# Optimization experiments

Measured on AMD Instinct MI355X. Metric: run time of the kernel, lower is better.

## Reference

```python
import jax, jax.numpy as jnp
from jax import lax
import numpy as np

B, T, I, H, O = 64, 4096, 128, 256, 1

def setup_inputs() -> dict:
    key = jax.random.key(0)
    ks = jax.random.split(key, 6)
    x = jax.random.normal(ks[0], (B, T, I), dtype=jnp.float32)
    # Linear params with torch-style fan_in init scale
    Wd = jax.random.uniform(ks[1], (H, I), jnp.float32, -1.0, 1.0) / np.sqrt(I)
    bd = jax.random.uniform(ks[2], (H,), jnp.float32, -1.0, 1.0) / np.sqrt(I)
    Wo = jax.random.uniform(ks[3], (O, H), jnp.float32, -1.0, 1.0) / np.sqrt(H)
    bo = jax.random.uniform(ks[4], (O,), jnp.float32, -1.0, 1.0) / np.sqrt(H)
    tau = jnp.ones((H,), jnp.float32) * 2.0
    return {"x": x, "Wd": Wd, "bd": bd, "Wo": Wo, "bo": bo, "tau": tau}

def reference(x, Wd, bd, Wo, bo, tau):
    # precompute dense projection for all timesteps: [B,T,H]
    cur = jnp.einsum('bti,hi->bth', x, Wd) + bd
    alpha = jax.nn.sigmoid(tau)  # [H], per-channel decay
    mem0 = jnp.zeros((x.shape[0], tau.shape[0]), dtype=x.dtype)

    def step(mem, c_t):  # c_t: [B,H]
        mem = alpha * mem + (1.0 - alpha) * c_t
        return mem, mem

    _, mems = lax.scan(step, mem0, jnp.swapaxes(cur, 0, 1))  # mems: [T,B,H]
    mems = jnp.swapaxes(mems, 0, 1)  # [B,T,H]
    out = jax.nn.sigmoid(jnp.einsum('bth,oh->bto', mems, Wo) + bo)  # [B,T,O]
    return out
```

## Files before the change

kernel.cpp:

```cpp
#include <hip/hip_runtime.h>
#include <hip/hip_bf16.h>
#include <math.h>

#define BB 64
#define TT 4096
#define II 128
#define HH 256
#define DD 64
#define LL 128
#define NC (TT/LL)

typedef __attribute__((ext_vector_type(8))) short short8;
typedef __attribute__((ext_vector_type(4))) float f32x4;

__device__ inline ushort f2b(float f) {
    __hip_bfloat16 h = __float2bfloat16(f);
    return *reinterpret_cast<ushort*>(&h);
}

__global__ __launch_bounds__(256) void k0_tables(
    const float* __restrict__ Wd, const float* __restrict__ bd,
    const float* __restrict__ Wo, const float* __restrict__ bo,
    const float* __restrict__ tau,
    ushort* __restrict__ U, float* __restrict__ ybias)
{
    __shared__ float pw[HH];
    __shared__ float wb[HH];
    __shared__ float red[II];
    const int tid = threadIdx.x;
    const int blk = blockIdx.x;

    if (blk < DD) {
        const int d = blk;
        {
            float a = 1.0f / (1.0f + expf(-tau[tid]));
            pw[tid] = Wo[tid] * (1.0f - a) * exp2f((float)d * log2f(a));
        }
        __syncthreads();
        const int i = tid & 127, p = tid >> 7;
        float s = 0.0f;
#pragma unroll 8
        for (int hh = 0; hh < 128; ++hh) {
            int h = p * 128 + hh;
            s += pw[h] * Wd[h * II + i];
        }
        if (p) red[i] = s;
        __syncthreads();
        if (!p) U[d * II + i] = f2b(s + red[i]);
    } else {
        {
            float a = 1.0f / (1.0f + expf(-tau[tid]));
            pw[tid] = log2f(a);
            wb[tid] = Wo[tid] * bd[tid];
        }
        __syncthreads();
        const int t = (blk - DD) * 16 + (tid >> 4);
        const int hp = tid & 15;
        float s = 0.0f;
#pragma unroll
        for (int hh = 0; hh < 16; ++hh) {
            int h = hp * 16 + hh;
            s += wb[h] * (1.0f - exp2f((float)(t + 1) * pw[h]));
        }
#pragma unroll
        for (int m = 1; m < 16; m <<= 1) s += __shfl_xor(s, m, 64);
        if (hp == 0) ybias[t] = s + bo[0];
    }
}

__global__ __launch_bounds__(512, 8) void k1_conv(
    const float* __restrict__ x, const ushort* __restrict__ U,
    const float* __restrict__ ybias,
    float* __restrict__ fix, float* __restrict__ spill,
    float* __restrict__ out)
{
    __shared__ __align__(16) char smem[34048];
    float* P    = reinterpret_cast<float*>(smem);
    float* psum = reinterpret_cast<float*>(smem + 33280);

    const int b = blockIdx.x >> 5, tc = blockIdx.x & 31;
    const int t0 = tc * LL;
    const int tid  = threadIdx.x;
    const int lane = tid & 63, w = tid >> 6;
    const int l15  = lane & 15, quad = lane >> 4;

    const float4* xg = reinterpret_cast<const float4*>(x + ((size_t)b * TT + t0) * II);
#pragma unroll
    for (int it = 0; it < 4; ++it) {
        int c = it * 512 + tid;
        int r = c >> 4, ib = c & 15;
        float4 v0 = xg[r * 32 + ib * 2];
        float4 v1 = xg[r * 32 + ib * 2 + 1];
        short8 pk;
        ushort* pu = reinterpret_cast<ushort*>(&pk);
        pu[0] = f2b(v0.x); pu[1] = f2b(v0.y); pu[2] = f2b(v0.z); pu[3] = f2b(v0.w);
        pu[4] = f2b(v1.x); pu[5] = f2b(v1.y); pu[6] = f2b(v1.z); pu[7] = f2b(v1.w);
        int byte = (r << 8) + (ib << 4);
        byte ^= (r & 7) << 4;
        *reinterpret_cast<short8*>(smem + byte) = pk;
    }
    __syncthreads();

    const int nt = w & 3, mg = w >> 2;
    f32x4 acc[4];
#pragma unroll
    for (int mi = 0; mi < 4; ++mi) acc[mi] = (f32x4){0.f, 0.f, 0.f, 0.f};
#pragma unroll
    for (int kt = 0; kt < 4; ++kt) {
        short8 bfrag = *reinterpret_cast<const short8*>(
            &U[(nt * 16 + l15) * II + kt * 32 + quad * 8]);
#pragma unroll
        for (int mi = 0; mi < 4; ++mi) {
            int row  = (mg * 4 + mi) * 16 + l15;
            int byte = (row << 8) + kt * 64 + quad * 16;
            byte ^= (row & 7) << 4;
            short8 afrag = *reinterpret_cast<const short8*>(smem + byte);
            acc[mi] = __builtin_amdgcn_mfma_f32_16x16x32_bf16(afrag, bfrag, acc[mi], 0, 0, 0);
        }
    }
    __syncthreads();

#pragma unroll
    for (int mi = 0; mi < 4; ++mi)
#pragma unroll
        for (int rr = 0; rr < 4; ++rr)
            P[((mg * 4 + mi) * 16 + quad * 4 + rr) * 65 + nt * 16 + l15] = acc[mi][rr];
    __syncthreads();

    const int g = tid >> 8;
    const int j = tid & 255;
    float part = 0.0f;
    if (j < 192) {
#pragma unroll
        for (int i = 0; i < 32; ++i) {
            int d = g * 32 + i;
            int r = j - d;
            int rc = r < 0 ? 0 : (r > 127 ? 127 : r);
            float v = P[rc * 65 + d];
            part += (r == rc) ? v : 0.0f;
        }
        if (g) psum[j] = part;
    }
    __syncthreads();
    if (!g && j < 192) {
        float tot = part + psum[j];
        if (j < 63) {
            fix[((size_t)b * NC + tc) * 64 + j] = tot;
        } else if (j < 128) {
            int t = t0 + j;
            float yb = ybias[t < 128 ? t : 127];
            out[(size_t)b * TT + t] = 1.0f / (1.0f + expf(-(tot + yb)));
        } else {
            spill[((size_t)b * NC + tc) * 64 + (j - 128)] = tot;
        }
    }
}

__global__ __launch_bounds__(256) void k2_out(
    const float* __restrict__ fix, const float* __restrict__ spill,
    const float* __restrict__ ybias, float* __restrict__ out)
{
    int idx = blockIdx.x * 256 + threadIdx.x;
    int j = idx & 63, tc = (idx >> 6) & 31, b = idx >> 11;
    if (j >= 63) return;
    float v = fix[((size_t)b * NC + tc) * 64 + j];
    if (tc) v += spill[((size_t)b * NC + tc - 1) * 64 + j];
    int t = tc * LL + j;
    v += ybias[t < 128 ? t : 127];
    out[(size_t)b * TT + t] = 1.0f / (1.0f + expf(-v));
}

extern "C" void kernel_launch(void* const* d_in, const int* in_sizes, int n_in,
                              void* d_out, int out_size, void* d_ws, size_t ws_size,
                              hipStream_t stream) {
    const float* x   = (const float*)d_in[0];
    const float* Wd  = (const float*)d_in[1];
    const float* bd  = (const float*)d_in[2];
    const float* Wo  = (const float*)d_in[3];
    const float* bo  = (const float*)d_in[4];
    const float* tau = (const float*)d_in[5];
    float* out = (float*)d_out;

    float* ws = (float*)d_ws;
    float*  ybias = ws;
    ushort* U     = (ushort*)(ws + 128);
    float*  fix   = ws + 128 + 4096;
    float*  spill = fix + BB * NC * 64;

    k0_tables<<<72, 256, 0, stream>>>(Wd, bd, Wo, bo, tau, U, ybias);
    k1_conv<<<BB * NC, 512, 0, stream>>>(x, U, ybias, fix, spill, out);
    k2_out<<<512, 256, 0, stream>>>(fix, spill, ybias, out);
}
```

Before: 213.6 us.

## Load x fragments directly to registers and reduce diagonals with LDS atomics

The conv kernel no longer stages the bf16 x tile in shared memory. Each wave loads its own 16-row A fragments straight from global memory into registers and loops over all four U column tiles. The staged P matrix and the diagonal gather pass are replaced by shared-memory atomicAdd into a 192-entry accumulator indexed by row+d. This removes LDS traffic and two barriers, but adds 16 LDS atomics per thread, and contention on those atomics could serialize.

```diff
diff --git a/kernel.cpp b/kernel.cpp
--- a/kernel.cpp
+++ b/kernel.cpp
@@ -74,9 +74,7 @@
     float* __restrict__ fix, float* __restrict__ spill,
     float* __restrict__ out)
 {
-    __shared__ __align__(16) char smem[34048];
-    float* P    = reinterpret_cast<float*>(smem);
-    float* psum = reinterpret_cast<float*>(smem + 33280);
+    __shared__ float yacc[192];
 
     const int b = blockIdx.x >> 5, tc = blockIdx.x & 31;
     const int t0 = tc * LL;
@@ -84,66 +82,44 @@
     const int lane = tid & 63, w = tid >> 6;
     const int l15  = lane & 15, quad = lane >> 4;
 
-    const float4* xg = reinterpret_cast<const float4*>(x + ((size_t)b * TT + t0) * II);
+    if (tid < 192) yacc[tid] = 0.0f;
+
+    const float* xr = x + ((size_t)b * TT + t0 + w * 16 + l15) * II + quad * 8;
+    short8 af[4];
 #pragma unroll
-    for (int it = 0; it < 4; ++it) {
-        int c = it * 512 + tid;
-        int r = c >> 4, ib = c & 15;
-        float4 v0 = xg[r * 32 + ib * 2];
-        float4 v1 = xg[r * 32 + ib * 2 + 1];
-        short8 pk;
-        ushort* pu = reinterpret_cast<ushort*>(&pk);
+    for (int kt = 0; kt < 4; ++kt) {
+        float4 v0 = *reinterpret_cast<const float4*>(xr + kt * 32);
+        float4 v1 = *reinterpret_cast<const float4*>(xr + kt * 32 + 4);
+        ushort* pu = reinterpret_cast<ushort*>(&af[kt]);
         pu[0] = f2b(v0.x); pu[1] = f2b(v0.y); pu[2] = f2b(v0.z); pu[3] = f2b(v0.w);
         pu[4] = f2b(v1.x); pu[5] = f2b(v1.y); pu[6] = f2b(v1.z); pu[7] = f2b(v1.w);
-        int byte = (r << 8) + (ib << 4);
-        byte ^= (r & 7) << 4;
-        *reinterpret_cast<short8*>(smem + byte) = pk;
     }
+
     __syncthreads();
 
-    const int nt = w & 3, mg = w >> 2;
     f32x4 acc[4];
 #pragma unroll
-    for (int mi = 0; mi < 4; ++mi) acc[mi] = (f32x4){0.f, 0.f, 0.f, 0.f};
+    for (int nt = 0; nt < 4; ++nt) acc[nt] = (f32x4){0.f, 0.f, 0.f, 0.f};
+    const ushort* Ub = U + (size_t)l15 * II + quad * 8;
 #pragma unroll
-    for (int kt = 0; kt < 4; ++kt) {
-        short8 bfrag = *reinterpret_cast<const short8*>(
-            &U[(nt * 16 + l15) * II + kt * 32 + quad * 8]);
+    for (int nt = 0; nt < 4; ++nt)
 #pragma unroll
-        for (int mi = 0; mi < 4; ++mi) {
-            int row  = (mg * 4 + mi) * 16 + l15;
-            int byte = (row << 8) + kt * 64 + quad * 16;
-            byte ^= (row & 7) << 4;
-            short8 afrag = *reinterpret_cast<const short8*>(smem + byte);
-            acc[mi] = __builtin_amdgcn_mfma_f32_16x16x32_bf16(afrag, bfrag, acc[mi], 0, 0, 0);
+        for (int kt = 0; kt < 4; ++kt) {
+            short8 bf = *reinterpret_cast<const short8*>(Ub + (nt * 16) * II + kt * 32);
+            acc[nt] = __builtin_amdgcn_mfma_f32_16x16x32_bf16(af[kt], bf, acc[nt], 0, 0, 0);
         }
-    }
+
+    const int jb = w * 16 + quad * 4 + l15;
+#pragma unroll
+    for (int nt = 0; nt < 4; ++nt)
+#pragma unroll
+        for (int rr = 0; rr < 4; ++rr)
+            atomicAdd(&yacc[jb + nt * 16 + rr], acc[nt][rr]);
     __syncthreads();
 
-#pragma unroll
-    for (int mi = 0; mi < 4; ++mi)
-#pragma unroll
-        for (int rr = 0; rr < 4; ++rr)
-            P[((mg * 4 + mi) * 16 + quad * 4 + rr) * 65 + nt * 16 + l15] = acc[mi][rr];
-    __syncthreads();
-
-    const int g = tid >> 8;
-    const int j = tid & 255;
-    float part = 0.0f;
-    if (j < 192) {
-#pragma unroll
-        for (int i = 0; i < 32; ++i) {
-            int d = g * 32 + i;
-            int r = j - d;
-            int rc = r < 0 ? 0 : (r > 127 ? 127 : r);
-            float v = P[rc * 65 + d];
-            part += (r == rc) ? v : 0.0f;
-        }
-        if (g) psum[j] = part;
-    }
-    __syncthreads();
-    if (!g && j < 192) {
-        float tot = part + psum[j];
+    if (tid < 191) {
+        const int j = tid;
+        float tot = yacc[j];
         if (j < 63) {
             fix[((size_t)b * NC + tc) * 64 + j] = tot;
         } else if (j < 128) {
```

Result: slower. 277.9 us (+30.1%).
